# Kernel tuning notes

Hardware: AMD Instinct MI355X
Metric: run time of the kernel (lower is better)

Reference implementation:

```python
import jax, jax.numpy as jnp
import numpy as np

UNITS = 256


def setup_inputs() -> dict:
    key = jax.random.key(0)
    ks = jax.random.split(key, 9)
    B, H, W, C = 8, 64, 64, UNITS
    x = jax.random.normal(ks[0], (B, H, W, C), dtype=jnp.float32)
    # 1x1 Conv2D == per-pixel linear: weight [C_in, C_out], bias [C_out]
    def lin(k):
        return jax.random.normal(k, (C, UNITS), dtype=jnp.float32) * (2.0 / C) ** 0.5
    return {
        "x": x,
        "wq": lin(ks[1]), "bq": jnp.zeros((UNITS,), jnp.float32),
        "wk": lin(ks[2]), "bk": jnp.zeros((UNITS,), jnp.float32),
        "wv": lin(ks[3]), "bv": jnp.zeros((UNITS,), jnp.float32),
        "wp": lin(ks[4]), "bp": jnp.zeros((UNITS,), jnp.float32),
    }


def reference(x, wq, bq, wk, bk, wv, bv, wp, bp):
    B, H, W, C = x.shape
    N = H * W
    scale = jnp.asarray(UNITS, jnp.float32) ** -0.5
    xf = x.reshape(B, N, C)  # 1x1 conv == matmul over channels
    q = xf @ wq + bq
    k = xf @ wk + bk
    v = xf @ wv + bv
    # (b,h,w,c)x(b,H,W,c)->(b,h,w,H,W) flattened to (b,N,N)
    scores = jnp.einsum('bnc,bmc->bnm', q, k) * scale
    attn = jax.nn.softmax(scores, axis=-1)
    out = jnp.einsum('bnm,bmc->bnc', attn, v)
    proj = out @ wp + bp
    return x + proj.reshape(B, H, W, UNITS)
```

## Files before the change

kernel.cpp:

```cpp
#include <hip/hip_runtime.h>


typedef _Float16 half8 __attribute__((ext_vector_type(8)));
typedef _Float16 half4 __attribute__((ext_vector_type(4)));
typedef float f32x4 __attribute__((ext_vector_type(4)));
typedef float f32x16 __attribute__((ext_vector_type(16)));
typedef unsigned int u32x4 __attribute__((ext_vector_type(4)));
typedef unsigned int u32x2 __attribute__((ext_vector_type(2)));

#define MFMA16(a, b, c) __builtin_amdgcn_mfma_f32_16x16x32_f16((a), (b), (c), 0, 0, 0)
#define MFMA32(a, b, c) __builtin_amdgcn_mfma_f32_32x32x16_f16((a), (b), (c), 0, 0, 0)

#if __has_builtin(__builtin_amdgcn_exp2f)
#define EXP2(x) __builtin_amdgcn_exp2f(x)
#else
#define EXP2(x) exp2f(x)
#endif

#define QSCALE 0.09016843898f
#define ESHIFT 11.5415603f

__device__ __forceinline__ void lds_load16(const void* g, void* l) {
    __builtin_amdgcn_global_load_lds(
        (const __attribute__((address_space(1))) unsigned int*)g,
        (__attribute__((address_space(3))) unsigned int*)l, 16, 0, 0);
}

__global__ __launch_bounds__(256)
void wt_prep(const float* __restrict__ w0, const float* __restrict__ w1,
             const float* __restrict__ w2, const float* __restrict__ w3,
             _Float16* __restrict__ outw)
{
    __shared__ _Float16 sT[64 * 72];
    const int z = blockIdx.z;
    const float* W = (z == 0) ? w0 : (z == 1) ? w1 : (z == 2) ? w2 : w3;
    _Float16* O = outw + z * 65536;
    const int kb = blockIdx.x * 64, nb = blockIdx.y * 64;
    const int t = threadIdx.x;
    const int r = t >> 4, c4 = (t & 15) * 4;
#pragma unroll
    for (int i = 0; i < 4; ++i) {
        f32x4 ld = *(const f32x4*)(W + (size_t)(kb + r + i * 16) * 256 + nb + c4);
#pragma unroll
        for (int j = 0; j < 4; ++j) sT[(c4 + j) * 72 + r + i * 16] = (_Float16)ld[j];
    }
    __syncthreads();
#pragma unroll
    for (int i = 0; i < 4; ++i) {
        int n = r + i * 16;
        *(u32x2*)&O[(size_t)(nb + n) * 256 + kb + c4] = *(const u32x2*)&sT[n * 72 + c4];
    }
}

__global__ __launch_bounds__(256)
void qkv_gemm(const float* __restrict__ x, const _Float16* __restrict__ wt,
              const float* __restrict__ bq, const float* __restrict__ bk,
              const float* __restrict__ bv,
              _Float16* __restrict__ qo, _Float16* __restrict__ ko,
              _Float16* __restrict__ vo)
{
    __shared__ _Float16 smem[4 * 2560];
    _Float16* sA = smem;

    const int tid  = threadIdx.x;
    const int w    = tid >> 6;
    const int lane = tid & 63;
    const int quad = lane >> 4;
    const int l16  = lane & 15;
    const int m0   = blockIdx.x * 64;
    const int n0   = blockIdx.y * 64;
    const int rS = tid >> 2, cS = (tid & 3) << 3;

    const float* ap = x + (size_t)(m0 + rS) * 256 + cS;
    f32x4 a0 = *(const f32x4*)ap, a1 = *(const f32x4*)(ap + 4);
    u32x4 bst[3];
#pragma unroll
    for (int o = 0; o < 3; ++o)
        bst[o] = *(const u32x4*)(wt + o * 65536 + (size_t)(n0 + rS) * 256 + cS);

    f32x4 zero4 = {0.f, 0.f, 0.f, 0.f};
    f32x4 acc[3][4];
#pragma unroll
    for (int o = 0; o < 3; ++o)
#pragma unroll
        for (int nt = 0; nt < 4; ++nt) acc[o][nt] = zero4;

    for (int it = 0; it < 8; ++it) {
        __syncthreads();
        half8 t;
#pragma unroll
        for (int j = 0; j < 4; ++j) { t[j] = (_Float16)a0[j]; t[j + 4] = (_Float16)a1[j]; }
        *(half8*)&sA[rS * 40 + cS] = t;
#pragma unroll
        for (int o = 0; o < 3; ++o)
            *(u32x4*)&smem[2560 * (o + 1) + rS * 40 + cS] = bst[o];
        __syncthreads();
        if (it < 7) {
            int k0 = (it + 1) * 32;
            const float* ap2 = x + (size_t)(m0 + rS) * 256 + k0 + cS;
            a0 = *(const f32x4*)ap2; a1 = *(const f32x4*)(ap2 + 4);
#pragma unroll
            for (int o = 0; o < 3; ++o)
                bst[o] = *(const u32x4*)(wt + o * 65536 + (size_t)(n0 + rS) * 256 + k0 + cS);
        }
        half8 af = *(const half8*)&sA[(16 * w + l16) * 40 + quad * 8];
#pragma unroll
        for (int o = 0; o < 3; ++o)
#pragma unroll
            for (int nt = 0; nt < 4; ++nt) {
                half8 bf = *(const half8*)&smem[2560 * (o + 1) + (nt * 16 + l16) * 40 + quad * 8];
                acc[o][nt] = MFMA16(af, bf, acc[o][nt]);
            }
    }

#pragma unroll
    for (int nt = 0; nt < 4; ++nt) {
#pragma unroll
        for (int reg = 0; reg < 4; ++reg) {
            int row = m0 + 16 * w + quad * 4 + reg;
            int col = n0 + nt * 16 + l16;
            qo[(size_t)row * 256 + col] = (_Float16)((acc[0][nt][reg] + bq[col]) * QSCALE);
            ko[(size_t)row * 256 + col] = (_Float16)(acc[1][nt][reg] + bk[col]);
        }
    }
    __syncthreads();
    _Float16* sT = smem;
#pragma unroll
    for (int nt = 0; nt < 4; ++nt)
#pragma unroll
        for (int reg = 0; reg < 4; ++reg)
            sT[(nt * 16 + l16) * 72 + 16 * w + quad * 4 + reg] =
                (_Float16)(acc[2][nt][reg] + bv[n0 + nt * 16 + l16]);
    __syncthreads();
    int ch = tid >> 2, po = (tid & 3) << 4;
    int bb = m0 >> 12, pix = m0 & 4095;
    _Float16* dst = vo + (size_t)bb * 1048576 + (size_t)(n0 + ch) * 4096 + pix + po;
    *(u32x4*)dst       = *(const u32x4*)&sT[ch * 72 + po];
    *(u32x4*)(dst + 8) = *(const u32x4*)&sT[ch * 72 + po + 8];
}

__global__ __launch_bounds__(256)
void proj_gemm(const _Float16* __restrict__ opart, const float* __restrict__ lpart,
               const _Float16* __restrict__ Wt, const float* __restrict__ bias,
               const float* __restrict__ resid, float* __restrict__ out)
{
    __shared__ _Float16 smem[2 * 2560];
    _Float16* sA = smem;
    _Float16* sB = smem + 2560;

    const int tid  = threadIdx.x;
    const int w    = tid >> 6;
    const int lane = tid & 63;
    const int quad = lane >> 4;
    const int l16  = lane & 15;
    const int m0   = blockIdx.x * 64;
    const int n0   = blockIdx.y * 64;
    const int rS = tid >> 2, cS = (tid & 3) << 3;

    const _Float16* o1p = opart;
    const _Float16* o2p = opart + 8388608;
    const int row = m0 + rS;
    const float inv = 1.0f / (lpart[row] + lpart[32768 + row]);

    u32x4 a1v = *(const u32x4*)(o1p + (size_t)row * 256 + cS);
    u32x4 a2v = *(const u32x4*)(o2p + (size_t)row * 256 + cS);
    u32x4 bst = *(const u32x4*)(Wt + (size_t)(n0 + rS) * 256 + cS);

    f32x4 zero4 = {0.f, 0.f, 0.f, 0.f};
    f32x4 acc[4] = {zero4, zero4, zero4, zero4};

    for (int it = 0; it < 8; ++it) {
        __syncthreads();
        {
            half8 h1 = *(half8*)&a1v, h2 = *(half8*)&a2v, t;
#pragma unroll
            for (int j = 0; j < 8; ++j)
                t[j] = (_Float16)(((float)h1[j] + (float)h2[j]) * inv);
            *(half8*)&sA[rS * 40 + cS] = t;
        }
        *(u32x4*)&sB[rS * 40 + cS] = bst;
        __syncthreads();
        if (it < 7) {
            int k0 = (it + 1) * 32;
            a1v = *(const u32x4*)(o1p + (size_t)row * 256 + k0 + cS);
            a2v = *(const u32x4*)(o2p + (size_t)row * 256 + k0 + cS);
            bst = *(const u32x4*)(Wt + (size_t)(n0 + rS) * 256 + k0 + cS);
        }
        half8 af = *(const half8*)&sA[(16 * w + l16) * 40 + quad * 8];
#pragma unroll
        for (int nt = 0; nt < 4; ++nt) {
            half8 bf = *(const half8*)&sB[(nt * 16 + l16) * 40 + quad * 8];
            acc[nt] = MFMA16(af, bf, acc[nt]);
        }
    }
#pragma unroll
    for (int nt = 0; nt < 4; ++nt) {
#pragma unroll
        for (int reg = 0; reg < 4; ++reg) {
            int orow = m0 + 16 * w + quad * 4 + reg;
            int col = n0 + nt * 16 + l16;
            out[(size_t)orow * 256 + col] =
                acc[nt][reg] + bias[col] + resid[(size_t)orow * 256 + col];
        }
    }
}

__global__ __launch_bounds__(256, 2)
void attn_kernel(const _Float16* __restrict__ q, const _Float16* __restrict__ k,
                 const _Float16* __restrict__ vt, _Float16* __restrict__ opart,
                 float* __restrict__ lpart)
{
    extern __shared__ char smem[];
    char* sKb = smem;
    char* sVb = smem + 32768;

    const int tid  = threadIdx.x;
    const int w    = tid >> 6;
    const int lane = tid & 63;
    const int l31  = lane & 31;
    const int hi   = lane >> 5;
    const int kh   = blockIdx.x & 1;
    const int qt   = (blockIdx.x >> 1) & 31;
    const int b    = blockIdx.x >> 6;

    char* sPw = smem + 65536 + w * 2560;

    const _Float16* kb = k  + (size_t)b * 1048576 + (size_t)kh * 524288;
    const _Float16* vb = vt + (size_t)b * 1048576 + kh * 2048;
    const int rowbase = qt * 128 + w * 32;

    half8 qf[16];
    {
        const _Float16* q0 = q + (size_t)(b * 4096 + rowbase + l31) * 256 + hi * 8;
#pragma unroll
        for (int s = 0; s < 16; ++s) qf[s] = *(const half8*)(q0 + s * 16);
    }

    f32x16 o[8];
#pragma unroll
    for (int i = 0; i < 8; ++i)
#pragma unroll
        for (int j = 0; j < 16; ++j) o[i][j] = 0.f;
    float ls = 0.f;

    const int koffL = l31 * 256 + hi * 8;

#pragma unroll
    for (int j = 0; j < 4; ++j) {
        int s = w * 4 + j;
        lds_load16(kb + koffL + s * 16, sKb + s * 1024);
        int ct = s >> 1, ks = s & 1;
        lds_load16(vb + (size_t)(32 * ct + l31) * 4096 + 16 * ks + 8 * hi,
                   sVb + s * 1024);
    }

    for (int kt = 0; kt < 64; ++kt) {
        const int p = kt & 1;
        __syncthreads();

        if (kt < 63) {
            const _Float16* ktb = kb + (size_t)(kt + 1) * 8192;
            const _Float16* vtb = vb + (kt + 1) * 32;
            char* dK = sKb + (1 - p) * 16384;
            char* dV = sVb + (1 - p) * 16384;
#pragma unroll
            for (int j = 0; j < 4; ++j) {
                int s = w * 4 + j;
                lds_load16(ktb + koffL + s * 16, dK + s * 1024);
                int ct = s >> 1, ks = s & 1;
                lds_load16(vtb + (size_t)(32 * ct + l31) * 4096 + 16 * ks + 8 * hi,
                           dV + s * 1024);
            }
        }

        const char* K = sKb + p * 16384;
        const char* V = sVb + p * 16384;

        f32x16 sacc;
#pragma unroll
        for (int j = 0; j < 16; ++j) sacc[j] = 0.f;
#pragma unroll
        for (int s = 0; s < 16; ++s) {
            half8 af = *(const half8*)(K + s * 1024 + lane * 16);
            sacc = MFMA32(af, qf[s], sacc);
        }

#pragma unroll
        for (int rb = 0; rb < 4; ++rb) {
            float p0 = EXP2(sacc[rb * 4 + 0] - ESHIFT);
            float p1 = EXP2(sacc[rb * 4 + 1] - ESHIFT);
            float p2 = EXP2(sacc[rb * 4 + 2] - ESHIFT);
            float p3 = EXP2(sacc[rb * 4 + 3] - ESHIFT);
            ls += (p0 + p1) + (p2 + p3);
            half4 t;
            t[0] = (_Float16)p0; t[1] = (_Float16)p1;
            t[2] = (_Float16)p2; t[3] = (_Float16)p3;
            *(half4*)(sPw + l31 * 80 + (8 * rb + 4 * hi) * 2) = t;
        }
        __asm__ volatile("s_waitcnt lgkmcnt(0)" ::: "memory");
        half8 pf0 = *(const half8*)(sPw + l31 * 80 + hi * 16);
        half8 pf1 = *(const half8*)(sPw + l31 * 80 + 32 + hi * 16);

#pragma unroll
        for (int ct = 0; ct < 8; ++ct) {
            half8 b0 = *(const half8*)(V + (ct * 2 + 0) * 1024 + lane * 16);
            half8 b1 = *(const half8*)(V + (ct * 2 + 1) * 1024 + lane * 16);
            o[ct] = MFMA32(pf0, b0, o[ct]);
            o[ct] = MFMA32(pf1, b1, o[ct]);
        }
    }

    ls += __shfl_xor(ls, 32);
    _Float16* po = opart + (size_t)kh * 8388608 + (size_t)(b * 4096 + rowbase) * 256;
    float* pl = lpart + kh * 32768 + b * 4096 + rowbase;
    if (hi == 0) pl[l31] = ls;
#pragma unroll
    for (int ct = 0; ct < 8; ++ct) {
#pragma unroll
        for (int reg = 0; reg < 16; ++reg) {
            int row = (reg & 3) + 8 * (reg >> 2) + 4 * hi;
            po[(size_t)row * 256 + ct * 32 + l31] = (_Float16)o[ct][reg];
        }
    }
}

extern "C" void kernel_launch(void* const* d_in, const int* in_sizes, int n_in,
                              void* d_out, int out_size, void* d_ws, size_t ws_size,
                              hipStream_t stream) {
    const float* x  = (const float*)d_in[0];
    const float* wq = (const float*)d_in[1];
    const float* bq = (const float*)d_in[2];
    const float* wk = (const float*)d_in[3];
    const float* bk = (const float*)d_in[4];
    const float* wv = (const float*)d_in[5];
    const float* bv = (const float*)d_in[6];
    const float* wp = (const float*)d_in[7];
    const float* bp = (const float*)d_in[8];

    _Float16* qws  = (_Float16*)d_ws;
    _Float16* kws  = qws + 8388608;
    _Float16* vtws = kws + 8388608;
    _Float16* ows  = vtws + 8388608;
    _Float16* wt   = ows + 16777216;
    float*    lws  = (float*)(wt + 262144);

    dim3 blk(256);

    (void)hipFuncSetAttribute((const void*)attn_kernel,
                              hipFuncAttributeMaxDynamicSharedMemorySize, 75776);

    wt_prep<<<dim3(4, 4, 4), blk, 0, stream>>>(wq, wk, wv, wp, wt);
    qkv_gemm<<<dim3(512, 4), blk, 0, stream>>>(x, wt, bq, bk, bv, qws, kws, vtws);
    attn_kernel<<<dim3(512), blk, 75776, stream>>>(qws, kws, vtws, ows, lws);
    proj_gemm<<<dim3(512, 4), blk, 0, stream>>>(ows, lws, wt + 196608, bp, x, (float*)d_out);
}
```

Measured before the change: 316.4 us.

## Double query rows per wave in attention and reorient QKV GEMM warp tiling

The attention kernel now gives each wave 64 query rows instead of 32. Each K and V fragment read from LDS feeds twice as many MFMAs, and the grid shrinks to 256 blocks with occupancy lowered to one block per CU and more LDS. Separately, the QKV GEMM swaps its warp tiling so each wave owns a 16-column slice across all 64 rows, reusing one B fragment over four A fragments. The trade-off is much higher register pressure (two sets of 16 query fragments and 16 output accumulators), lower occupancy, and only 256 blocks, which may underfill a 256-CU device.

After: 306.2 us. -3.2%, faster.

```diff
diff --git a/kernel.cpp b/kernel.cpp
--- a/kernel.cpp
+++ b/kernel.cpp
@@ -83,7 +83,7 @@
 #pragma unroll
     for (int o = 0; o < 3; ++o)
 #pragma unroll
-        for (int nt = 0; nt < 4; ++nt) acc[o][nt] = zero4;
+        for (int mt = 0; mt < 4; ++mt) acc[o][mt] = zero4;
 
     for (int it = 0; it < 8; ++it) {
         __syncthreads();
@@ -103,34 +103,37 @@
             for (int o = 0; o < 3; ++o)
                 bst[o] = *(const u32x4*)(wt + o * 65536 + (size_t)(n0 + rS) * 256 + k0 + cS);
         }
-        half8 af = *(const half8*)&sA[(16 * w + l16) * 40 + quad * 8];
-#pragma unroll
-        for (int o = 0; o < 3; ++o)
-#pragma unroll
-            for (int nt = 0; nt < 4; ++nt) {
-                half8 bf = *(const half8*)&smem[2560 * (o + 1) + (nt * 16 + l16) * 40 + quad * 8];
-                acc[o][nt] = MFMA16(af, bf, acc[o][nt]);
-            }
-    }
-
-#pragma unroll
-    for (int nt = 0; nt < 4; ++nt) {
+        half8 af[4];
+#pragma unroll
+        for (int mt = 0; mt < 4; ++mt)
+            af[mt] = *(const half8*)&sA[(mt * 16 + l16) * 40 + quad * 8];
+#pragma unroll
+        for (int o = 0; o < 3; ++o) {
+            half8 bf = *(const half8*)&smem[2560 * (o + 1) + (16 * w + l16) * 40 + quad * 8];
+#pragma unroll
+            for (int mt = 0; mt < 4; ++mt)
+                acc[o][mt] = MFMA16(af[mt], bf, acc[o][mt]);
+        }
+    }
+
+    const int col = n0 + 16 * w + l16;
+#pragma unroll
+    for (int mt = 0; mt < 4; ++mt) {
 #pragma unroll
         for (int reg = 0; reg < 4; ++reg) {
-            int row = m0 + 16 * w + quad * 4 + reg;
-            int col = n0 + nt * 16 + l16;
-            qo[(size_t)row * 256 + col] = (_Float16)((acc[0][nt][reg] + bq[col]) * QSCALE);
-            ko[(size_t)row * 256 + col] = (_Float16)(acc[1][nt][reg] + bk[col]);
+            int row = m0 + 16 * mt + quad * 4 + reg;
+            qo[(size_t)row * 256 + col] = (_Float16)((acc[0][mt][reg] + bq[col]) * QSCALE);
+            ko[(size_t)row * 256 + col] = (_Float16)(acc[1][mt][reg] + bk[col]);
         }
     }
     __syncthreads();
     _Float16* sT = smem;
 #pragma unroll
-    for (int nt = 0; nt < 4; ++nt)
+    for (int mt = 0; mt < 4; ++mt)
 #pragma unroll
         for (int reg = 0; reg < 4; ++reg)
-            sT[(nt * 16 + l16) * 72 + 16 * w + quad * 4 + reg] =
-                (_Float16)(acc[2][nt][reg] + bv[n0 + nt * 16 + l16]);
+            sT[(16 * w + l16) * 72 + 16 * mt + quad * 4 + reg] =
+                (_Float16)(acc[2][mt][reg] + bv[col]);
     __syncthreads();
     int ch = tid >> 2, po = (tid & 3) << 4;
     int bb = m0 >> 12, pix = m0 & 4095;
@@ -205,7 +208,7 @@
     }
 }
 
-__global__ __launch_bounds__(256, 2)
+__global__ __launch_bounds__(256, 1)
 void attn_kernel(const _Float16* __restrict__ q, const _Float16* __restrict__ k,
                  const _Float16* __restrict__ vt, _Float16* __restrict__ opart,
                  float* __restrict__ lpart)
@@ -220,28 +223,32 @@
     const int l31  = lane & 31;
     const int hi   = lane >> 5;
     const int kh   = blockIdx.x & 1;
-    const int qt   = (blockIdx.x >> 1) & 31;
-    const int b    = blockIdx.x >> 6;
-
-    char* sPw = smem + 65536 + w * 2560;
+    const int qg   = (blockIdx.x >> 1) & 15;
+    const int b    = blockIdx.x >> 5;
+
+    char* sPw = smem + 65536 + w * 5120;
 
     const _Float16* kb = k  + (size_t)b * 1048576 + (size_t)kh * 524288;
     const _Float16* vb = vt + (size_t)b * 1048576 + kh * 2048;
-    const int rowbase = qt * 128 + w * 32;
-
-    half8 qf[16];
+    const int rowbase = qg * 256 + w * 64;
+
+    half8 qf0[16], qf1[16];
     {
         const _Float16* q0 = q + (size_t)(b * 4096 + rowbase + l31) * 256 + hi * 8;
-#pragma unroll
-        for (int s = 0; s < 16; ++s) qf[s] = *(const half8*)(q0 + s * 16);
-    }
-
-    f32x16 o[8];
+        const _Float16* q1 = q0 + 32 * 256;
+#pragma unroll
+        for (int s = 0; s < 16; ++s) {
+            qf0[s] = *(const half8*)(q0 + s * 16);
+            qf1[s] = *(const half8*)(q1 + s * 16);
+        }
+    }
+
+    f32x16 o0[8], o1[8];
 #pragma unroll
     for (int i = 0; i < 8; ++i)
 #pragma unroll
-        for (int j = 0; j < 16; ++j) o[i][j] = 0.f;
-    float ls = 0.f;
+        for (int j = 0; j < 16; ++j) { o0[i][j] = 0.f; o1[i][j] = 0.f; }
+    float ls0 = 0.f, ls1 = 0.f;
 
     const int koffL = l31 * 256 + hi * 8;
 
@@ -276,50 +283,67 @@
         const char* K = sKb + p * 16384;
         const char* V = sVb + p * 16384;
 
-        f32x16 sacc;
-#pragma unroll
-        for (int j = 0; j < 16; ++j) sacc[j] = 0.f;
+        f32x16 sa0, sa1;
+#pragma unroll
+        for (int j = 0; j < 16; ++j) { sa0[j] = 0.f; sa1[j] = 0.f; }
 #pragma unroll
         for (int s = 0; s < 16; ++s) {
             half8 af = *(const half8*)(K + s * 1024 + lane * 16);
-            sacc = MFMA32(af, qf[s], sacc);
+            sa0 = MFMA32(af, qf0[s], sa0);
+            sa1 = MFMA32(af, qf1[s], sa1);
         }
 
 #pragma unroll
         for (int rb = 0; rb < 4; ++rb) {
-            float p0 = EXP2(sacc[rb * 4 + 0] - ESHIFT);
-            float p1 = EXP2(sacc[rb * 4 + 1] - ESHIFT);
-            float p2 = EXP2(sacc[rb * 4 + 2] - ESHIFT);
-            float p3 = EXP2(sacc[rb * 4 + 3] - ESHIFT);
-            ls += (p0 + p1) + (p2 + p3);
+            float p0 = EXP2(sa0[rb * 4 + 0] - ESHIFT);
+            float p1 = EXP2(sa0[rb * 4 + 1] - ESHIFT);
+            float p2 = EXP2(sa0[rb * 4 + 2] - ESHIFT);
+            float p3 = EXP2(sa0[rb * 4 + 3] - ESHIFT);
+            ls0 += (p0 + p1) + (p2 + p3);
             half4 t;
             t[0] = (_Float16)p0; t[1] = (_Float16)p1;
             t[2] = (_Float16)p2; t[3] = (_Float16)p3;
             *(half4*)(sPw + l31 * 80 + (8 * rb + 4 * hi) * 2) = t;
+
+            float r0 = EXP2(sa1[rb * 4 + 0] - ESHIFT);
+            float r1 = EXP2(sa1[rb * 4 + 1] - ESHIFT);
+            float r2 = EXP2(sa1[rb * 4 + 2] - ESHIFT);
+            float r3 = EXP2(sa1[rb * 4 + 3] - ESHIFT);
+            ls1 += (r0 + r1) + (r2 + r3);
+            half4 u;
+            u[0] = (_Float16)r0; u[1] = (_Float16)r1;
+            u[2] = (_Float16)r2; u[3] = (_Float16)r3;
+            *(half4*)(sPw + (32 + l31) * 80 + (8 * rb + 4 * hi) * 2) = u;
         }
         __asm__ volatile("s_waitcnt lgkmcnt(0)" ::: "memory");
-        half8 pf0 = *(const half8*)(sPw + l31 * 80 + hi * 16);
-        half8 pf1 = *(const half8*)(sPw + l31 * 80 + 32 + hi * 16);
+        half8 pf00 = *(const half8*)(sPw + l31 * 80 + hi * 16);
+        half8 pf01 = *(const half8*)(sPw + l31 * 80 + 32 + hi * 16);
+        half8 pf10 = *(const half8*)(sPw + (32 + l31) * 80 + hi * 16);
+        half8 pf11 = *(const half8*)(sPw + (32 + l31) * 80 + 32 + hi * 16);
 
 #pragma unroll
         for (int ct = 0; ct < 8; ++ct) {
             half8 b0 = *(const half8*)(V + (ct * 2 + 0) * 1024 + lane * 16);
             half8 b1 = *(const half8*)(V + (ct * 2 + 1) * 1024 + lane * 16);
-            o[ct] = MFMA32(pf0, b0, o[ct]);
-            o[ct] = MFMA32(pf1, b1, o[ct]);
-        }
-    }
-
-    ls += __shfl_xor(ls, 32);
+            o0[ct] = MFMA32(pf00, b0, o0[ct]);
+            o0[ct] = MFMA32(pf01, b1, o0[ct]);
+            o1[ct] = MFMA32(pf10, b0, o1[ct]);
+            o1[ct] = MFMA32(pf11, b1, o1[ct]);
+        }
+    }
+
+    ls0 += __shfl_xor(ls0, 32);
+    ls1 += __shfl_xor(ls1, 32);
     _Float16* po = opart + (size_t)kh * 8388608 + (size_t)(b * 4096 + rowbase) * 256;
     float* pl = lpart + kh * 32768 + b * 4096 + rowbase;
-    if (hi == 0) pl[l31] = ls;
+    if (hi == 0) { pl[l31] = ls0; pl[32 + l31] = ls1; }
 #pragma unroll
     for (int ct = 0; ct < 8; ++ct) {
 #pragma unroll
         for (int reg = 0; reg < 16; ++reg) {
             int row = (reg & 3) + 8 * (reg >> 2) + 4 * hi;
-            po[(size_t)row * 256 + ct * 32 + l31] = (_Float16)o[ct][reg];
+            po[(size_t)row * 256 + ct * 32 + l31] = (_Float16)o0[ct][reg];
+            po[(size_t)(32 + row) * 256 + ct * 32 + l31] = (_Float16)o1[ct][reg];
         }
     }
 }
@@ -347,10 +371,10 @@
     dim3 blk(256);
 
     (void)hipFuncSetAttribute((const void*)attn_kernel,
-                              hipFuncAttributeMaxDynamicSharedMemorySize, 75776);
+                              hipFuncAttributeMaxDynamicSharedMemorySize, 86016);
 
     wt_prep<<<dim3(4, 4, 4), blk, 0, stream>>>(wq, wk, wv, wp, wt);
     qkv_gemm<<<dim3(512, 4), blk, 0, stream>>>(x, wt, bq, bk, bv, qws, kws, vtws);
-    attn_kernel<<<dim3(512), blk, 75776, stream>>>(qws, kws, vtws, ows, lws);
+    attn_kernel<<<dim3(256), blk, 86016, stream>>>(qws, kws, vtws, ows, lws);
     proj_gemm<<<dim3(512, 4), blk, 0, stream>>>(ows, lws, wt + 196608, bp, x, (float*)d_out);
 }
```
